# Performance work log

Measured on AMD Instinct MI355X. Metric: run time of the kernel, lower is better.

The kernel has to match this reference:

```python
import jax, jax.numpy as jnp
import numpy as np

I, H, B, T = 17, 128, 32768, 19

def setup_inputs() -> dict:
    key = jax.random.key(0)
    ks = jax.random.split(key, 7)
    s = 1.0 / np.sqrt(H)  # PyTorch LSTMCell/Linear init scale
    u = lambda k, shape: jax.random.uniform(k, shape, jnp.float32, -s, s)
    return {
        "x": jax.random.normal(ks[0], (B, T, I), jnp.float32),
        "W_ih": u(ks[1], (4 * H, I)),
        "W_hh": u(ks[2], (4 * H, H)),
        "b_ih": u(ks[3], (4 * H,)),
        "b_hh": u(ks[4], (4 * H,)),
        "W_out": u(ks[5], (I, H)),
        "b_out": u(ks[6], (I,)),
    }

def reference(x, W_ih, W_hh, b_ih, b_hh, W_out, b_out):
    B_, T_, _ = x.shape
    Hh = W_hh.shape[1]
    # Precompute input projections for all timesteps in one GEMM: [B,T,4H]
    x_proj = jnp.einsum('bti,gi->btg', x, W_ih) + b_ih + b_hh

    def step(carry, xp_t):
        h, c = carry
        gates = xp_t + h @ W_hh.T            # [B,4H]
        i_g, f_g, g_g, o_g = jnp.split(gates, 4, axis=-1)
        c = jax.nn.sigmoid(f_g) * c + jax.nn.sigmoid(i_g) * jnp.tanh(g_g)
        h = jax.nn.sigmoid(o_g) * jnp.tanh(c)
        y = h @ W_out.T + b_out              # [B,I]
        return (h, c), y

    h0 = jnp.zeros((B_, Hh), x.dtype)
    c0 = jnp.zeros((B_, Hh), x.dtype)
    _, ys = jax.lax.scan(step, (h0, c0), jnp.swapaxes(x_proj, 0, 1))  # ys: [T,B,I]
    return jnp.swapaxes(ys, 0, 1)  # [B,T,I]
```

## Files before the change

kernel.cpp:

```cpp
#include <hip/hip_runtime.h>

#define I_DIM 17
#define H_DIM 128
#define T_DIM 19
#define B_DIM 32768
#define M_ROWS 128
#define NTHR 512
#define GRID (B_DIM / M_ROWS)
#define XI 323
#define NF (M_ROWS * XI)
#define XSLOT 4352

#define OFF_H 0
#define OFF_X 65536
#define LDS_TOT 148224

typedef __bf16 bf16x8 __attribute__((ext_vector_type(8)));
typedef float f32x4 __attribute__((ext_vector_type(4)));
union FragU { bf16x8 v; unsigned short s[8]; uint4 u; };

#define K1 1.4426950408889634f
#define K2 2.8853900817779268f

__device__ __forceinline__ unsigned short f2bf(float f) {
    union { float f; unsigned u; } x; x.f = f;
    return (unsigned short)((x.u + 0x8000u) >> 16);
}

#define HALF_BODY(T_, P_, HF_, YPT_) do {                                         \
    f32x4 acc[4][4];                                                              \
    _Pragma("unroll") for (int mtl = 0; mtl < 4; ++mtl)                           \
        _Pragma("unroll") for (int g = 0; g < 4; ++g)                             \
            acc[mtl][g] = (f32x4){bias[g], bias[g], bias[g], bias[g]};            \
    \
    _Pragma("unroll") for (int mtl = 0; mtl < 4; ++mtl) {                         \
        FragU fx; fx.u = (uint4){0u, 0u, 0u, 0u};                                 \
        if (q < 2)                                                                \
            fx.v = *(const bf16x8*)(smem + xyA + ((HF_) * 4 + mtl) * 512);        \
        else if (q == 2)                                                          \
            fx.s[0] = *(const unsigned short*)(smem + xk16 + ((HF_) * 4 + mtl) * 32); \
        _Pragma("unroll") for (int g = 0; g < 4; ++g)                             \
            acc[mtl][g] = __builtin_amdgcn_mfma_f32_16x16x32_bf16(fx.v, wihr[g], acc[mtl][g], 0, 0, 0); \
    }                                                                             \
                          \
    _Pragma("unroll") for (int kk = 0; kk < 4; ++kk)                              \
        _Pragma("unroll") for (int mtl = 0; mtl < 4; ++mtl) {                     \
            bf16x8 a = *(const bf16x8*)(smem + vkk[kk] + ((1 - (P_)) * 32768 + ((HF_) * 4 + mtl) * 4096)); \
            _Pragma("unroll") for (int g = 0; g < 4; ++g)                         \
                acc[mtl][g] = __builtin_amdgcn_mfma_f32_16x16x32_bf16(a, whh[kk][g], acc[mtl][g], 0, 0, 0); \
        }                                                                         \
                               \
    if ((T_) > 0) {                                                               \
        f32x4 ya = {0.f, 0.f, 0.f, 0.f};                                          \
        _Pragma("unroll") for (int kk = 0; kk < 4; ++kk) {                        \
            bf16x8 a = *(const bf16x8*)(smem + vkk[kk] + vyk + ((1 - (P_)) * 32768 + (HF_) * 16384)); \
            ya = __builtin_amdgcn_mfma_f32_16x16x32_bf16(a, wor[kk], ya, 0, 0, 0);\
        }                                                                         \
        if (yok) {                                                                \
            _Pragma("unroll") for (int r = 0; r < 4; ++r)                         \
                YPT_[r * XI] = ya[r] + ybo;                                       \
        }                                                                         \
        YPT_ += I_DIM;                                                            \
    }                                                                             \
                      \
    _Pragma("unroll") for (int mtl = 0; mtl < 4; ++mtl)                           \
        _Pragma("unroll") for (int r = 0; r < 4; ++r) {                           \
            float ig = acc[mtl][0][r], fg = acc[mtl][1][r];                       \
            float gg = acc[mtl][2][r], og = acc[mtl][3][r];                       \
            float ui = __builtin_amdgcn_exp2f(-K1 * ig);                          \
            float uf = __builtin_amdgcn_exp2f(-K1 * fg);                          \
            float vg = __builtin_amdgcn_exp2f(-K2 * gg);                          \
            float uo = __builtin_amdgcn_exp2f(-K1 * og);                          \
            float A_ = 1.f + ui, F_ = 1.f + uf, G_ = 1.f + vg;                    \
            float AG = A_ * G_;                                                   \
            float c = (cst[(HF_) * 16 + mtl * 4 + r] * AG + (1.f - vg) * F_) * __builtin_amdgcn_rcpf(F_ * AG); \
            cst[(HF_) * 16 + mtl * 4 + r] = c;                                    \
            float vc = __builtin_amdgcn_exp2f(-K2 * c);                           \
            float h = (1.f - vc) * __builtin_amdgcn_rcpf((1.f + uo) * (1.f + vc));\
            *(unsigned short*)(smem + vwr[r] + ((P_) * 32768 + ((HF_) * 4 + mtl) * 4096)) = f2bf(h); \
        }                                                                         \
} while (0)

#define STEP(T_, P_) do {                  \
    HALF_BODY(T_, P_, 0, ypt0);            \
    HALF_BODY(T_, P_, 1, ypt1);            \
    xyA += XSLOT; xk16 += XSLOT;           \
    __syncthreads();                       \
} while (0)

__global__ __launch_bounds__(NTHR)
__attribute__((amdgpu_waves_per_eu(2, 2)))
void flowlstm(
    const float* __restrict__ x, const float* __restrict__ W_ih,
    const float* __restrict__ W_hh, const float* __restrict__ b_ih,
    const float* __restrict__ b_hh, const float* __restrict__ W_out,
    const float* __restrict__ b_out, float* __restrict__ out)
{
    __shared__ __align__(16) unsigned char smem[LDS_TOT];
    const int tid = threadIdx.x;
    const int w = tid >> 6, lane = tid & 63, l15 = lane & 15, q = lane >> 4;
    const int cg = w;
    const int b0 = blockIdx.x * M_ROWS;

    #pragma unroll
    for (int j = 0; j < 16; ++j)
        *(unsigned*)(smem + 32768 + (unsigned)(tid + j * NTHR) * 4) = 0u;

    {
        const float* xb = x + (size_t)b0 * XI;
        for (int j = 0; j < 81; ++j) {
            int f = tid + j * NTHR;
            if (f < NF) {
                float v = xb[f];
                unsigned uf_ = (unsigned)f;
                unsigned row = (uf_ * 51943u) >> 24;
                unsigned s = uf_ - row * 323u;
                unsigned t = (s * 61681u) >> 20;
                unsigned k = s - t * 17u;
                unsigned a;
                if (k == 16) a = OFF_X + t * XSLOT + 4096 + row * 2;
                else a = OFF_X + t * XSLOT + (row >> 4) * 512 + (k >> 3) * 256
                       + (row & 15) * 16 + (k & 7) * 2;
                *(unsigned short*)(smem + a) = f2bf(v);
            }
        }
    }
    bf16x8 whh[4][4];
    #pragma unroll
    for (int kk = 0; kk < 4; ++kk)
        #pragma unroll
        for (int g = 0; g < 4; ++g) {
            int n = g * H_DIM + cg * 16 + l15;
            const float* s = W_hh + n * H_DIM + kk * 32 + q * 8;
            FragU fu;
            #pragma unroll
            for (int e = 0; e < 8; ++e) fu.s[e] = f2bf(s[e]);
            whh[kk][g] = fu.v;
        }
    bf16x8 wihr[4];
    #pragma unroll
    for (int g = 0; g < 4; ++g) {
        int n = g * H_DIM + cg * 16 + l15;
        FragU fu;
        #pragma unroll
        for (int e = 0; e < 8; ++e) {
            int k = q * 8 + e;
            fu.s[e] = (k < I_DIM) ? f2bf(W_ih[n * I_DIM + k]) : (unsigned short)0;
        }
        wihr[g] = fu.v;
    }
    const int ymt = w >> 1, yct = w & 1;
    const int ycol = yct * 16 + l15;
    bf16x8 wor[4];
    #pragma unroll
    for (int kk = 0; kk < 4; ++kk) {
        FragU fu;
        #pragma unroll
        for (int e = 0; e < 8; ++e)
            fu.s[e] = (ycol < I_DIM) ? f2bf(W_out[ycol * H_DIM + kk * 32 + q * 8 + e])
                                     : (unsigned short)0;
        wor[kk] = fu.v;
    }
    float bias[4];
    #pragma unroll
    for (int g = 0; g < 4; ++g) {
        int col = g * H_DIM + cg * 16 + l15;
        bias[g] = b_ih[col] + b_hh[col];
    }
    const unsigned xr7 = (unsigned)((l15 & 7) << 4);
    unsigned vkk[4], vwr[4];
    #pragma unroll
    for (int kk = 0; kk < 4; ++kk)
        vkk[kk] = (unsigned)(l15 * 256 + ((kk * 64 + q * 16) ^ xr7));
    const int colh2 = (cg * 16 + l15) * 2;
    #pragma unroll
    for (int r = 0; r < 4; ++r) {
        int rq = q * 4 + r;
        vwr[r] = (unsigned)(rq * 256 + (colh2 ^ ((rq & 7) << 4)));
    }
    const unsigned vyk = (unsigned)(ymt * 4096);
    const bool yok = (ycol < I_DIM);
    const float ybo = b_out[ycol < I_DIM ? ycol : 16];
    unsigned xyA  = (unsigned)(OFF_X + (q < 2 ? q * 256 : 0) + l15 * 16);
    unsigned xk16 = (unsigned)(OFF_X + 4096 + l15 * 2);
    float* ypt0 = out + (size_t)(b0 + ymt * 16 + q * 4) * XI + ycol;
    float* ypt1 = ypt0 + (size_t)64 * XI;

    float cst[32];
    #pragma unroll
    for (int i = 0; i < 32; ++i) cst[i] = 0.f;

    __syncthreads();

    #pragma unroll 1
    for (int t = 0; t < T_DIM - 1; t += 2) {
        STEP(t, 0);
        STEP(t + 1, 1);
    }
    STEP(T_DIM - 1, 0);

    {
        f32x4 ya = {0.f, 0.f, 0.f, 0.f};
        #pragma unroll
        for (int kk = 0; kk < 4; ++kk) {
            bf16x8 a = *(const bf16x8*)(smem + vkk[kk] + vyk);
            ya = __builtin_amdgcn_mfma_f32_16x16x32_bf16(a, wor[kk], ya, 0, 0, 0);
        }
        if (yok) {
            #pragma unroll
            for (int r = 0; r < 4; ++r)
                ypt0[r * XI] = ya[r] + ybo;
        }
    }
    {
        f32x4 ya = {0.f, 0.f, 0.f, 0.f};
        #pragma unroll
        for (int kk = 0; kk < 4; ++kk) {
            bf16x8 a = *(const bf16x8*)(smem + vkk[kk] + vyk + 16384);
            ya = __builtin_amdgcn_mfma_f32_16x16x32_bf16(a, wor[kk], ya, 0, 0, 0);
        }
        if (yok) {
            #pragma unroll
            for (int r = 0; r < 4; ++r)
                ypt1[r * XI] = ya[r] + ybo;
        }
    }
}

extern "C" void kernel_launch(void* const* d_in, const int* in_sizes, int n_in,
                              void* d_out, int out_size, void* d_ws, size_t ws_size,
                              hipStream_t stream) {
    const float* x     = (const float*)d_in[0];
    const float* W_ih  = (const float*)d_in[1];
    const float* W_hh  = (const float*)d_in[2];
    const float* b_ih  = (const float*)d_in[3];
    const float* b_hh  = (const float*)d_in[4];
    const float* W_out = (const float*)d_in[5];
    const float* b_out = (const float*)d_in[6];
    float* out = (float*)d_out;

    dim3 grid(GRID), block(NTHR);
    flowlstm<<<grid, block, 0, stream>>>(x, W_ih, W_hh, b_ih, b_hh, W_out, b_out, out);
}
```

Measured before the change: 170.5 us.

## Software-pipeline LSTM step into quarter tiles overlapping MFMA with gate math

Each timestep is split into four quarter tiles with two alternating accumulator sets, so the MFMA work for one quarter is issued while the previous quarter's sigmoid/tanh math runs. The gate scale factors (-log2e, -2log2e) are folded into W_ih, W_hh and the biases, which removes the per-element multiplies before exp2. Step 0 is peeled to skip the recurrent matmul because h0 is zero, which also drops the zero-initialisation of the h buffer. The output projection is merged into one burst per step. This raises register pressure (two accumulator sets) and applies the bf16 rounding to pre-scaled weights.

```diff
diff --git a/kernel.cpp b/kernel.cpp
--- a/kernel.cpp
+++ b/kernel.cpp
@@ -27,63 +27,74 @@
     return (unsigned short)((x.u + 0x8000u) >> 16);
 }
 
-#define HALF_BODY(T_, P_, HF_, YPT_) do {                                         \
-    f32x4 acc[4][4];                                                              \
-    _Pragma("unroll") for (int mtl = 0; mtl < 4; ++mtl)                           \
+
+#define MFMA_Q(P_, QT_, ACC_, REC_) do {                                          \
+    _Pragma("unroll") for (int m2 = 0; m2 < 2; ++m2) {                            \
         _Pragma("unroll") for (int g = 0; g < 4; ++g)                             \
-            acc[mtl][g] = (f32x4){bias[g], bias[g], bias[g], bias[g]};            \
-    \
-    _Pragma("unroll") for (int mtl = 0; mtl < 4; ++mtl) {                         \
+            ACC_[m2][g] = (f32x4){bias[g], bias[g], bias[g], bias[g]};            \
         FragU fx; fx.u = (uint4){0u, 0u, 0u, 0u};                                 \
         if (q < 2)                                                                \
-            fx.v = *(const bf16x8*)(smem + xyA + ((HF_) * 4 + mtl) * 512);        \
+            fx.v = *(const bf16x8*)(smem + xyA + ((QT_) * 2 + m2) * 512);         \
         else if (q == 2)                                                          \
-            fx.s[0] = *(const unsigned short*)(smem + xk16 + ((HF_) * 4 + mtl) * 32); \
+            fx.s[0] = *(const unsigned short*)(smem + xk16 + ((QT_) * 2 + m2) * 32); \
         _Pragma("unroll") for (int g = 0; g < 4; ++g)                             \
-            acc[mtl][g] = __builtin_amdgcn_mfma_f32_16x16x32_bf16(fx.v, wihr[g], acc[mtl][g], 0, 0, 0); \
-    }                                                                             \
-                          \
-    _Pragma("unroll") for (int kk = 0; kk < 4; ++kk)                              \
-        _Pragma("unroll") for (int mtl = 0; mtl < 4; ++mtl) {                     \
-            bf16x8 a = *(const bf16x8*)(smem + vkk[kk] + ((1 - (P_)) * 32768 + ((HF_) * 4 + mtl) * 4096)); \
-            _Pragma("unroll") for (int g = 0; g < 4; ++g)                         \
-                acc[mtl][g] = __builtin_amdgcn_mfma_f32_16x16x32_bf16(a, whh[kk][g], acc[mtl][g], 0, 0, 0); \
-        }                                                                         \
-                               \
-    if ((T_) > 0) {                                                               \
-        f32x4 ya = {0.f, 0.f, 0.f, 0.f};                                          \
-        _Pragma("unroll") for (int kk = 0; kk < 4; ++kk) {                        \
-            bf16x8 a = *(const bf16x8*)(smem + vkk[kk] + vyk + ((1 - (P_)) * 32768 + (HF_) * 16384)); \
-            ya = __builtin_amdgcn_mfma_f32_16x16x32_bf16(a, wor[kk], ya, 0, 0, 0);\
-        }                                                                         \
-        if (yok) {                                                                \
-            _Pragma("unroll") for (int r = 0; r < 4; ++r)                         \
-                YPT_[r * XI] = ya[r] + ybo;                                       \
-        }                                                                         \
-        YPT_ += I_DIM;                                                            \
-    }                                                                             \
-                      \
-    _Pragma("unroll") for (int mtl = 0; mtl < 4; ++mtl)                           \
+            ACC_[m2][g] = __builtin_amdgcn_mfma_f32_16x16x32_bf16(fx.v, wihr[g], ACC_[m2][g], 0, 0, 0); \
+    }                                                                             \
+    if (REC_) {                                                                   \
+        _Pragma("unroll") for (int kk = 0; kk < 4; ++kk)                          \
+            _Pragma("unroll") for (int m2 = 0; m2 < 2; ++m2) {                    \
+                bf16x8 a = *(const bf16x8*)(smem + vkk[kk] + ((1 - (P_)) * 32768 + ((QT_) * 2 + m2) * 4096)); \
+                _Pragma("unroll") for (int g = 0; g < 4; ++g)                     \
+                    ACC_[m2][g] = __builtin_amdgcn_mfma_f32_16x16x32_bf16(a, whh[kk][g], ACC_[m2][g], 0, 0, 0); \
+            }                                                                     \
+    }                                                                             \
+} while (0)
+
+#define ELEM_Q(P_, QT_, ACC_) do {                                                \
+    _Pragma("unroll") for (int m2 = 0; m2 < 2; ++m2)                              \
         _Pragma("unroll") for (int r = 0; r < 4; ++r) {                           \
-            float ig = acc[mtl][0][r], fg = acc[mtl][1][r];                       \
-            float gg = acc[mtl][2][r], og = acc[mtl][3][r];                       \
-            float ui = __builtin_amdgcn_exp2f(-K1 * ig);                          \
-            float uf = __builtin_amdgcn_exp2f(-K1 * fg);                          \
-            float vg = __builtin_amdgcn_exp2f(-K2 * gg);                          \
-            float uo = __builtin_amdgcn_exp2f(-K1 * og);                          \
+            float ui = __builtin_amdgcn_exp2f(ACC_[m2][0][r]);                    \
+            float uf = __builtin_amdgcn_exp2f(ACC_[m2][1][r]);                    \
+            float vg = __builtin_amdgcn_exp2f(ACC_[m2][2][r]);                    \
+            float uo = __builtin_amdgcn_exp2f(ACC_[m2][3][r]);                    \
             float A_ = 1.f + ui, F_ = 1.f + uf, G_ = 1.f + vg;                    \
             float AG = A_ * G_;                                                   \
-            float c = (cst[(HF_) * 16 + mtl * 4 + r] * AG + (1.f - vg) * F_) * __builtin_amdgcn_rcpf(F_ * AG); \
-            cst[(HF_) * 16 + mtl * 4 + r] = c;                                    \
+            int ci = (QT_) * 8 + m2 * 4 + r;                                      \
+            float c = (cst[ci] * AG + (1.f - vg) * F_) * __builtin_amdgcn_rcpf(F_ * AG); \
+            cst[ci] = c;                                                          \
             float vc = __builtin_amdgcn_exp2f(-K2 * c);                           \
             float h = (1.f - vc) * __builtin_amdgcn_rcpf((1.f + uo) * (1.f + vc));\
-            *(unsigned short*)(smem + vwr[r] + ((P_) * 32768 + ((HF_) * 4 + mtl) * 4096)) = f2bf(h); \
+            *(unsigned short*)(smem + vwr[r] + ((P_) * 32768 + ((QT_) * 2 + m2) * 4096)) = f2bf(h); \
         }                                                                         \
 } while (0)
 
-#define STEP(T_, P_) do {                  \
-    HALF_BODY(T_, P_, 0, ypt0);            \
-    HALF_BODY(T_, P_, 1, ypt1);            \
+#define Y_BURST(P_) do {                                                          \
+    f32x4 ya0 = {0.f, 0.f, 0.f, 0.f}, ya1 = {0.f, 0.f, 0.f, 0.f};                 \
+    _Pragma("unroll") for (int kk = 0; kk < 4; ++kk) {                            \
+        bf16x8 a0 = *(const bf16x8*)(smem + vkk[kk] + vyk + (1 - (P_)) * 32768);  \
+        bf16x8 a1 = *(const bf16x8*)(smem + vkk[kk] + vyk + (1 - (P_)) * 32768 + 16384); \
+        ya0 = __builtin_amdgcn_mfma_f32_16x16x32_bf16(a0, wor[kk], ya0, 0, 0, 0); \
+        ya1 = __builtin_amdgcn_mfma_f32_16x16x32_bf16(a1, wor[kk], ya1, 0, 0, 0); \
+    }                                                                             \
+    if (yok) {                                                                    \
+        _Pragma("unroll") for (int r = 0; r < 4; ++r) {                           \
+            ypt0[r * XI] = ya0[r] + ybo;                                          \
+            ypt1[r * XI] = ya1[r] + ybo;                                          \
+        }                                                                         \
+    }                                                                             \
+    ypt0 += I_DIM; ypt1 += I_DIM;                                                 \
+} while (0)
+
+#define STEP(P_) do {                      \
+    MFMA_Q(P_, 0, accA, 1);                \
+    MFMA_Q(P_, 1, accB, 1);                \
+    ELEM_Q(P_, 0, accA);                   \
+    MFMA_Q(P_, 2, accA, 1);                \
+    ELEM_Q(P_, 1, accB);                   \
+    MFMA_Q(P_, 3, accB, 1);                \
+    ELEM_Q(P_, 2, accA);                   \
+    Y_BURST(P_);                           \
+    ELEM_Q(P_, 3, accB);                   \
     xyA += XSLOT; xk16 += XSLOT;           \
     __syncthreads();                       \
 } while (0)
@@ -101,10 +112,6 @@
     const int w = tid >> 6, lane = tid & 63, l15 = lane & 15, q = lane >> 4;
     const int cg = w;
     const int b0 = blockIdx.x * M_ROWS;
-
-    #pragma unroll
-    for (int j = 0; j < 16; ++j)
-        *(unsigned*)(smem + 32768 + (unsigned)(tid + j * NTHR) * 4) = 0u;
 
     {
         const float* xb = x + (size_t)b0 * XI;
@@ -125,6 +132,8 @@
             }
         }
     }
+    float gsc[4] = { -K1, -K1, -K2, -K1 };
+
     bf16x8 whh[4][4];
     #pragma unroll
     for (int kk = 0; kk < 4; ++kk)
@@ -134,7 +143,7 @@
             const float* s = W_hh + n * H_DIM + kk * 32 + q * 8;
             FragU fu;
             #pragma unroll
-            for (int e = 0; e < 8; ++e) fu.s[e] = f2bf(s[e]);
+            for (int e = 0; e < 8; ++e) fu.s[e] = f2bf(s[e] * gsc[g]);
             whh[kk][g] = fu.v;
         }
     bf16x8 wihr[4];
@@ -145,7 +154,7 @@
         #pragma unroll
         for (int e = 0; e < 8; ++e) {
             int k = q * 8 + e;
-            fu.s[e] = (k < I_DIM) ? f2bf(W_ih[n * I_DIM + k]) : (unsigned short)0;
+            fu.s[e] = (k < I_DIM) ? f2bf(W_ih[n * I_DIM + k] * gsc[g]) : (unsigned short)0;
         }
         wihr[g] = fu.v;
     }
@@ -165,7 +174,7 @@
     #pragma unroll
     for (int g = 0; g < 4; ++g) {
         int col = g * H_DIM + cg * 16 + l15;
-        bias[g] = b_ih[col] + b_hh[col];
+        bias[g] = (b_ih[col] + b_hh[col]) * gsc[g];
     }
     const unsigned xr7 = (unsigned)((l15 & 7) << 4);
     unsigned vkk[4], vwr[4];
@@ -190,39 +199,42 @@
     #pragma unroll
     for (int i = 0; i < 32; ++i) cst[i] = 0.f;
 
+    f32x4 accA[2][4], accB[2][4];
+
     __syncthreads();
 
+    MFMA_Q(0, 0, accA, 0);
+    MFMA_Q(0, 1, accB, 0);
+    ELEM_Q(0, 0, accA);
+    MFMA_Q(0, 2, accA, 0);
+    ELEM_Q(0, 1, accB);
+    MFMA_Q(0, 3, accB, 0);
+    ELEM_Q(0, 2, accA);
+    ELEM_Q(0, 3, accB);
+    xyA += XSLOT; xk16 += XSLOT;
+    __syncthreads();
+
     #pragma unroll 1
-    for (int t = 0; t < T_DIM - 1; t += 2) {
-        STEP(t, 0);
-        STEP(t + 1, 1);
-    }
-    STEP(T_DIM - 1, 0);
+    for (int t = 1; t < T_DIM; t += 2) {
+        STEP(1);
+        STEP(0);
+    }
 
     {
-        f32x4 ya = {0.f, 0.f, 0.f, 0.f};
+        f32x4 ya0 = {0.f, 0.f, 0.f, 0.f}, ya1 = {0.f, 0.f, 0.f, 0.f};
         #pragma unroll
         for (int kk = 0; kk < 4; ++kk) {
-            bf16x8 a = *(const bf16x8*)(smem + vkk[kk] + vyk);
-            ya = __builtin_amdgcn_mfma_f32_16x16x32_bf16(a, wor[kk], ya, 0, 0, 0);
+            bf16x8 a0 = *(const bf16x8*)(smem + vkk[kk] + vyk);
+            bf16x8 a1 = *(const bf16x8*)(smem + vkk[kk] + vyk + 16384);
+            ya0 = __builtin_amdgcn_mfma_f32_16x16x32_bf16(a0, wor[kk], ya0, 0, 0, 0);
+            ya1 = __builtin_amdgcn_mfma_f32_16x16x32_bf16(a1, wor[kk], ya1, 0, 0, 0);
         }
         if (yok) {
             #pragma unroll
-            for (int r = 0; r < 4; ++r)
-                ypt0[r * XI] = ya[r] + ybo;
-        }
-    }
-    {
-        f32x4 ya = {0.f, 0.f, 0.f, 0.f};
-        #pragma unroll
-        for (int kk = 0; kk < 4; ++kk) {
-            bf16x8 a = *(const bf16x8*)(smem + vkk[kk] + vyk + 16384);
-            ya = __builtin_amdgcn_mfma_f32_16x16x32_bf16(a, wor[kk], ya, 0, 0, 0);
-        }
-        if (yok) {
-            #pragma unroll
-            for (int r = 0; r < 4; ++r)
-                ypt1[r * XI] = ya[r] + ybo;
+            for (int r = 0; r < 4; ++r) {
+                ypt0[r * XI] = ya0[r] + ybo;
+                ypt1[r * XI] = ya1[r] + ybo;
+            }
         }
     }
 }
```

Measured after the change: 160.5 us. -5.9%, faster.
